# Performance work log

Hardware: AMD Instinct MI355X
Metric: run time of the kernel (lower is better)

The kernel has to match this reference:

```python
import jax, jax.numpy as jnp
import numpy as np

D_MODEL = 1024
D_FFN = 2048
WINDOW = 64
EPS = 1e-6


def rmsnorm(x, w):
    rms = jnp.sqrt(jnp.mean(x * x, axis=-1, keepdims=True) + EPS)
    return x / rms * w


def setup_inputs() -> dict:
    key = jax.random.key(0)
    ks = jax.random.split(key, 9)
    s = 0.02
    return {
        "x": jax.random.normal(ks[0], (4, 2048, D_MODEL), dtype=jnp.float32),
        "norm1_w": jnp.ones((D_MODEL,), dtype=jnp.float32),
        "norm2_w": jnp.ones((D_MODEL,), dtype=jnp.float32),
        "Wq": jax.random.normal(ks[1], (D_MODEL, D_MODEL), dtype=jnp.float32) * s,
        "Wk": jax.random.normal(ks[2], (D_MODEL, D_MODEL), dtype=jnp.float32) * s,
        "Wv": jax.random.normal(ks[3], (D_MODEL, D_MODEL), dtype=jnp.float32) * s,
        "Wo": jax.random.normal(ks[4], (D_MODEL, D_MODEL), dtype=jnp.float32) * s,
        "W1": jax.random.normal(ks[5], (D_MODEL, D_FFN), dtype=jnp.float32) * s,
        "W2": jax.random.normal(ks[6], (D_FFN, D_MODEL), dtype=jnp.float32) * s,
        "W3": jax.random.normal(ks[7], (D_MODEL, D_FFN), dtype=jnp.float32) * s,
    }


def reference(x, norm1_w, norm2_w, Wq, Wk, Wv, Wo, W1, W2, W3):
    B, T, D = x.shape
    scale = D ** (-0.5)
    residual = x
    xn = rmsnorm(x, norm1_w)
    q = xn @ Wq  # [B,T,D]
    k = xn @ Wk
    v = xn @ Wv
    # causal local-window mask: attend iff 0 <= i-j < WINDOW
    rows = jnp.arange(T)[:, None]
    cols = jnp.arange(T)[None, :]
    mask = (cols <= rows) & (rows - cols < WINDOW)  # [T,T] bool
    scores = jnp.einsum("bid,bjd->bij", q, k) * scale
    scores = jnp.where(mask[None], scores, -jnp.inf)
    weights = jax.nn.softmax(scores, axis=-1)
    attended = jnp.einsum("bij,bjd->bid", weights, v)
    x = residual + attended @ Wo
    # SwiGLU FFN
    xn2 = rmsnorm(x, norm2_w)
    ffn = (jax.nn.silu(xn2 @ W1) * (xn2 @ W3)) @ W2
    return x + ffn
```

## Files before the change

kernel.cpp:

```cpp
#include <hip/hip_runtime.h>
#include <hip/hip_bf16.h>

typedef __attribute__((ext_vector_type(8))) short bf16x8;
typedef __attribute__((ext_vector_type(4))) float f32x4;

__device__ __forceinline__ short to_bf16s(float f) {
    union { __hip_bfloat16 h; short s; } u;
    u.h = __float2bfloat16(f);
    return u.s;
}

__device__ __forceinline__ float bf16s_to_f(short s) {
    union { float f; unsigned u; } cv;
    cv.u = ((unsigned)(unsigned short)s) << 16;
    return cv.f;
}

__device__ __forceinline__ void load_lds16(const void* g, void* l) {
    __builtin_amdgcn_global_load_lds((const __attribute__((address_space(1))) void*)g,
                                     (__attribute__((address_space(3))) void*)l, 16, 0, 0);
}

__global__ __launch_bounds__(256)
void transpose_all(const float* __restrict__ Wq, const float* __restrict__ Wk,
                   const float* __restrict__ Wv, const float* __restrict__ Wo,
                   const float* __restrict__ W1, const float* __restrict__ W3,
                   const float* __restrict__ W2,
                   short* __restrict__ WqT, short* __restrict__ WkT,
                   short* __restrict__ WvT, short* __restrict__ WoT,
                   short* __restrict__ W1T, short* __restrict__ W3T,
                   short* __restrict__ W2T) {
    __shared__ float tile[32][33];
    const int bid = blockIdx.x;
    const float* src; short* dst; int K, N, tl;
    if (bid < 4096) {
        const int wi = bid >> 10; tl = bid & 1023;
        src = wi == 0 ? Wq : wi == 1 ? Wk : wi == 2 ? Wv : Wo;
        dst = wi == 0 ? WqT : wi == 1 ? WkT : wi == 2 ? WvT : WoT;
        K = 1024; N = 1024;
    } else if (bid < 8192) {
        const int wi = (bid - 4096) >> 11; tl = (bid - 4096) & 2047;
        src = wi ? W3 : W1; dst = wi ? W3T : W1T;
        K = 1024; N = 2048;
    } else {
        tl = bid - 8192; src = W2; dst = W2T;
        K = 2048; N = 1024;
    }
    const int nx = N >> 5;
    const int n0 = (tl % nx) * 32, k0 = (tl / nx) * 32;
    const int t = threadIdx.x;
    {
        const int lr = t >> 3, lc = (t & 7) * 4;
        float4 v = *(const float4*)&src[(long)(k0 + lr) * N + n0 + lc];
        tile[lr][lc] = v.x; tile[lr][lc + 1] = v.y;
        tile[lr][lc + 2] = v.z; tile[lr][lc + 3] = v.w;
    }
    __syncthreads();
    {
        const int nr = t >> 3, kc = (t & 7) * 4;
        short4 o;
        o.x = to_bf16s(tile[kc][nr]);
        o.y = to_bf16s(tile[kc + 1][nr]);
        o.z = to_bf16s(tile[kc + 2][nr]);
        o.w = to_bf16s(tile[kc + 3][nr]);
        *(short4*)&dst[(long)(n0 + nr) * K + k0 + kc] = o;
    }
}

__global__ __launch_bounds__(256)
void rmsnorm_kernel(const float* __restrict__ x, const float* __restrict__ wt,
                    short* __restrict__ out) {
    const int D = 1024;
    const long row = blockIdx.x;
    const int t = threadIdx.x;
    float4 v = ((const float4*)(x + row * D))[t];
    float ss = v.x * v.x + v.y * v.y + v.z * v.z + v.w * v.w;
    #pragma unroll
    for (int off = 32; off; off >>= 1) ss += __shfl_xor(ss, off);
    __shared__ float red[4];
    if ((t & 63) == 0) red[t >> 6] = ss;
    __syncthreads();
    ss = red[0] + red[1] + red[2] + red[3];
    const float inv = rsqrtf(ss * (1.0f / 1024.0f) + 1e-6f);
    float4 wv = ((const float4*)wt)[t];
    short4 o;
    o.x = to_bf16s(v.x * inv * wv.x);
    o.y = to_bf16s(v.y * inv * wv.y);
    o.z = to_bf16s(v.z * inv * wv.z);
    o.w = to_bf16s(v.w * inv * wv.w);
    *(short4*)&out[row * D + t * 4] = o;
}

#define MFMA16(MB, NB, BREG)                                                   \
    __builtin_amdgcn_s_barrier();                                              \
    asm volatile("s_waitcnt lgkmcnt(0)" ::: "memory");                         \
    __builtin_amdgcn_sched_barrier(0);                                         \
    __builtin_amdgcn_s_setprio(1);                                             \
    _Pragma("unroll")                                                          \
    for (int m_ = 0; m_ < 4; ++m_)                                             \
        _Pragma("unroll")                                                      \
        for (int n_ = 0; n_ < 2; ++n_) {                                       \
            acc[(MB) + m_][(NB) + n_] = __builtin_amdgcn_mfma_f32_16x16x32_bf16( \
                a[m_][0], BREG[n_][0], acc[(MB) + m_][(NB) + n_], 0, 0, 0);    \
            acc[(MB) + m_][(NB) + n_] = __builtin_amdgcn_mfma_f32_16x16x32_bf16( \
                a[m_][1], BREG[n_][1], acc[(MB) + m_][(NB) + n_], 0, 0, 0);    \
        }                                                                      \
    __builtin_amdgcn_s_setprio(0);                                             \
    __builtin_amdgcn_s_barrier();

#define READA(BUF, MG)                                                         \
    _Pragma("unroll")                                                          \
    for (int m_ = 0; m_ < 4; ++m_) {                                           \
        const int rih_ = ((MG) * 4 + m_) * 16 + lm;                            \
        const int rb_ = ((BUF) * 2 + wr) * 16384 + rih_ * 128;                 \
        a[m_][0] = *(const bf16x8*)&lds[rb_ + ((lk * 16) ^ sw)];               \
        a[m_][1] = *(const bf16x8*)&lds[rb_ + ((64 + lk * 16) ^ sw)];          \
    }

#define READB(BUF, NH, ARR)                                                    \
    _Pragma("unroll")                                                          \
    for (int n_ = 0; n_ < 2; ++n_) {                                           \
        const int rih_ = (wc & 1) * 64 + ((NH) * 2 + n_) * 16 + lm;            \
        const int rb_ = 65536 + ((BUF) * 2 + (wc >> 1)) * 16384 + rih_ * 128;  \
        ARR[n_][0] = *(const bf16x8*)&lds[rb_ + ((lk * 16) ^ sw)];             \
        ARR[n_][1] = *(const bf16x8*)&lds[rb_ + ((64 + lk * 16) ^ sw)];        \
    }

template<int EPI>
__global__ __launch_bounds__(512, 2)
void gemm256(const short* __restrict__ A, const short* __restrict__ B0,
             const short* __restrict__ aux, const float* __restrict__ res,
             void* __restrict__ outp, short* __restrict__ outp2,
             int M, int N, int K) {
    __shared__ __align__(16) char lds[131072];

    const int t = threadIdx.x;
    const int lane = t & 63, w = t >> 6;
    const int wr = w >> 2, wc = w & 3;
    const int lm = lane & 15, lk = lane >> 4;
    const int sw = (lm & 7) << 4;

    const int nbn = N >> 8;
    const int nwg = gridDim.x;
    const int chunk = nwg >> 3;
    const int logical = (blockIdx.x & 7) * chunk + (blockIdx.x >> 3);
    const int bm = logical / nbn, bn = logical - (logical / nbn) * nbn;

    const long Kb = (long)K * 2;
    const char* Ab = (const char*)A;
    const char* Bb = (const char*)B0;

    long srcA[2][2], srcB[2][2];
    {
        const int rowp = t >> 3;
        const int cbx = (t & 7) * 16;
        const int swz = ((t >> 3) & 7) << 4;
        #pragma unroll
        for (int h = 0; h < 2; ++h)
            #pragma unroll
            for (int c = 0; c < 2; ++c) {
                srcA[h][c] = (long)(bm * 256 + h * 128 + c * 64 + rowp) * Kb + (cbx ^ swz);
                srcB[h][c] = (long)(bn * 256 + h * 128 + c * 64 + rowp) * Kb + (cbx ^ swz);
            }
    }
    auto stA = [&](int kt, int h) {
        const int buf = kt & 1;
        #pragma unroll
        for (int c = 0; c < 2; ++c)
            load_lds16(Ab + srcA[h][c] + (long)kt * 128,
                       &lds[(buf * 2 + h) * 16384 + c * 8192 + t * 16]);
    };
    auto stB = [&](int kt, int h) {
        const int buf = kt & 1;
        #pragma unroll
        for (int c = 0; c < 2; ++c)
            load_lds16(Bb + srcB[h][c] + (long)kt * 128,
                       &lds[65536 + (buf * 2 + h) * 16384 + c * 8192 + t * 16]);
    };

    f32x4 acc[8][4] = {};
    bf16x8 a[4][2], b0[2][2], b1[2][2];
    const int nt = K >> 6;

    stB(0, 0); stB(0, 1); stA(0, 0); stA(0, 1); stB(1, 0); stB(1, 1);
    asm volatile("s_waitcnt vmcnt(4)" ::: "memory");
    __builtin_amdgcn_s_barrier();

    for (int kt0 = 0; kt0 < nt; kt0 += 2) {
        const int kt1 = kt0 + 1;
        const bool pf = (kt0 + 2) < nt;

        READA(0, 0); READB(0, 0, b0);
        stA(kt1, 0);
        MFMA16(0, 0, b0)
        READB(0, 1, b1);
        stA(kt1, 1);
        MFMA16(0, 2, b1)
        READA(0, 1);
        if (pf) stB(kt0 + 2, 0);
        MFMA16(4, 2, b1)
        if (pf) { stB(kt0 + 2, 1); asm volatile("s_waitcnt vmcnt(4)" ::: "memory"); }
        else    { asm volatile("s_waitcnt vmcnt(0)" ::: "memory"); }
        MFMA16(4, 0, b0)
        READA(1, 0); READB(1, 0, b0);
        if (pf) stA(kt0 + 2, 0);
        MFMA16(0, 0, b0)
        READB(1, 1, b1);
        if (pf) stA(kt0 + 2, 1);
        MFMA16(0, 2, b1)
        READA(1, 1);
        if (pf) stB(kt1 + 2, 0);
        MFMA16(4, 2, b1)
        if (pf) { stB(kt1 + 2, 1); asm volatile("s_waitcnt vmcnt(4)" ::: "memory"); }
        else    { asm volatile("s_waitcnt vmcnt(0)" ::: "memory"); }
        MFMA16(4, 0, b0)
    }

    #pragma unroll
    for (int mf = 0; mf < 8; ++mf)
      #pragma unroll
      for (int nf = 0; nf < 4; ++nf)
        #pragma unroll
        for (int r = 0; r < 4; ++r) {
            const int grow = bm * 256 + wr * 128 + mf * 16 + lk * 4 + r;
            const int gcol = bn * 256 + wc * 64 + nf * 16 + lm;
            const float v = acc[mf][nf][r];
            if constexpr (EPI == 0) {
                ((short*)outp)[(long)grow * N + gcol] = to_bf16s(v);
            } else if constexpr (EPI == 2) {
                const long i = (long)grow * N + gcol;
                ((float*)outp)[i] = res[i] + v;
            } else if constexpr (EPI == 4) {
                const long i = (long)grow * N + gcol;
                const float g = bf16s_to_f(aux[i]);
                const float sws = g / (1.f + __expf(-g));
                ((short*)outp)[i] = to_bf16s(sws * v);
            } else {
                if (gcol < 2048)
                    ((short*)outp)[(long)grow * 2048 + gcol] = to_bf16s(v);
                else
                    outp2[(long)(gcol - 2048) * 8192 + grow] = to_bf16s(v);
            }
        }
}

__global__ __launch_bounds__(128)
void attn_kernel(const short* __restrict__ Q, const short* __restrict__ Km,
                 int ldq, const short* __restrict__ VT, short* __restrict__ att) {
    const int T = 2048, D = 1024, Mtot = 8192;
    const int bid = blockIdx.x;
    const int b = bid >> 6;
    const int q0 = (bid & 63) << 5;
    const long qrow0 = (long)b * T + q0;
    const int t = threadIdx.x, lane = t & 63, w = t >> 6;

    __shared__ short Qs[32 * 32];
    __shared__ short Ks[96 * 32];
    __shared__ float S_lds[32][100];
    __shared__ short P_lds[32 * 96];
    __shared__ short VTs[128 * 96];

    f32x4 s[6] = {};
    const int trow = t >> 2, tk8 = (t & 3) * 8;
    for (int kt = 0; kt < 32; ++kt) {
        const int k0 = kt << 5;
        load_lds16(Q + (qrow0 + trow) * ldq + k0 + tk8, &Qs[t * 8]);
        #pragma unroll
        for (int s2 = 0; s2 < 3; ++s2) {
            const int krow = s2 * 32 + trow;
            int j = q0 - 64 + krow; if (j < 0) j = 0;
            load_lds16(Km + ((long)b * T + j) * ldq + k0 + tk8, &Ks[(s2 * 128 + t) * 8]);
        }
        __syncthreads();
        const int ko = (lane >> 4) * 8;
        const bf16x8 aq = *(const bf16x8*)&Qs[(w * 16 + (lane & 15)) * 32 + ko];
        #pragma unroll
        for (int n = 0; n < 6; ++n) {
            const bf16x8 bk = *(const bf16x8*)&Ks[(n * 16 + (lane & 15)) * 32 + ko];
            s[n] = __builtin_amdgcn_mfma_f32_16x16x32_bf16(aq, bk, s[n], 0, 0, 0);
        }
        __syncthreads();
    }
    #pragma unroll
    for (int n = 0; n < 6; ++n)
        #pragma unroll
        for (int r = 0; r < 4; ++r)
            S_lds[w * 16 + ((lane >> 4) << 2) + r][n * 16 + (lane & 15)] = s[n][r] * 0.03125f;
    __syncthreads();

    {
        const int row = t >> 2, c0 = (t & 3) * 24;
        float e[24];
        float mx = -1e30f;
        #pragma unroll
        for (int c = 0; c < 24; ++c) {
            const int kj = c0 + c;
            const bool valid = (kj > row) && (kj <= row + 64) && (q0 - 64 + kj >= 0);
            const float sv = valid ? S_lds[row][kj] : -1e30f;
            e[c] = sv;
            mx = fmaxf(mx, sv);
        }
        mx = fmaxf(mx, __shfl_xor(mx, 1));
        mx = fmaxf(mx, __shfl_xor(mx, 2));
        float sum = 0.f;
        #pragma unroll
        for (int c = 0; c < 24; ++c) {
            const float ev = (e[c] > -1e29f) ? __expf(e[c] - mx) : 0.f;
            e[c] = ev; sum += ev;
        }
        sum += __shfl_xor(sum, 1);
        sum += __shfl_xor(sum, 2);
        const float inv = 1.f / sum;
        #pragma unroll
        for (int c = 0; c < 24; ++c)
            P_lds[row * 96 + c0 + c] = to_bf16s(e[c] * inv);
    }
    __syncthreads();

    bf16x8 pa[3];
    {
        const int ko = (lane >> 4) * 8;
        #pragma unroll
        for (int kc = 0; kc < 3; ++kc)
            pa[kc] = *(const bf16x8*)&P_lds[(w * 16 + (lane & 15)) * 96 + kc * 32 + ko];
    }
    for (int dc = 0; dc < 8; ++dc) {
        #pragma unroll
        for (int s2 = 0; s2 < 12; ++s2) {
            const int idx = s2 * 128 + t;
            const int dr = idx / 12, c = idx - dr * 12;
            int j = q0 - 64 + c * 8; if (j < 0) j = 0;
            load_lds16(VT + (long)(dc * 128 + dr) * Mtot + b * T + j, &VTs[idx * 8]);
        }
        __syncthreads();
        f32x4 o[8] = {};
        const int ko = (lane >> 4) * 8;
        #pragma unroll
        for (int kc = 0; kc < 3; ++kc)
            #pragma unroll
            for (int n = 0; n < 8; ++n) {
                const bf16x8 vb = *(const bf16x8*)&VTs[(n * 16 + (lane & 15)) * 96 + kc * 32 + ko];
                o[n] = __builtin_amdgcn_mfma_f32_16x16x32_bf16(pa[kc], vb, o[n], 0, 0, 0);
            }
        __syncthreads();
        #pragma unroll
        for (int n = 0; n < 8; ++n)
            #pragma unroll
            for (int r = 0; r < 4; ++r) {
                const long grow = qrow0 + w * 16 + ((lane >> 4) << 2) + r;
                const int gcol = dc * 128 + n * 16 + (lane & 15);
                att[grow * D + gcol] = to_bf16s(o[n][r]);
            }
    }
}

extern "C" void kernel_launch(void* const* d_in, const int* in_sizes, int n_in,
                              void* d_out, int out_size, void* d_ws, size_t ws_size,
                              hipStream_t stream) {
    const float* x   = (const float*)d_in[0];
    const float* n1w = (const float*)d_in[1];
    const float* n2w = (const float*)d_in[2];
    const float* Wq  = (const float*)d_in[3];
    const float* Wk  = (const float*)d_in[4];
    const float* Wv  = (const float*)d_in[5];
    const float* Wo  = (const float*)d_in[6];
    const float* W1  = (const float*)d_in[7];
    const float* W2  = (const float*)d_in[8];
    const float* W3  = (const float*)d_in[9];

    const int M = 8192;
    char* ws = (char*)d_ws;
    size_t off = 0;
    auto alloc = [&](size_t bytes) { void* p = ws + off; off += (bytes + 255) & ~(size_t)255; return p; };

    short* xn1 = (short*)alloc((size_t)M * 1024 * 2);
    short* qk  = (short*)alloc((size_t)M * 2048 * 2);
    short* vT  = (short*)alloc((size_t)M * 1024 * 2);
    float* x2  = (float*)alloc((size_t)M * 1024 * 4);
    short* WqT = (short*)alloc((size_t)1024 * 1024 * 2);
    short* WkT = (short*)alloc((size_t)1024 * 1024 * 2);
    short* WvT = (short*)alloc((size_t)1024 * 1024 * 2);
    short* WoT = (short*)alloc((size_t)1024 * 1024 * 2);
    short* W1T = (short*)alloc((size_t)2048 * 1024 * 2);
    short* W3T = (short*)alloc((size_t)2048 * 1024 * 2);
    short* W2T = (short*)alloc((size_t)1024 * 2048 * 2);
    short* att = xn1;
    short* xn2 = qk;
    short* g1  = qk + (size_t)M * 1024;

    transpose_all<<<10240, 256, 0, stream>>>(Wq, Wk, Wv, Wo, W1, W3, W2,
                                             WqT, WkT, WvT, WoT, W1T, W3T, W2T);

    rmsnorm_kernel<<<M, 256, 0, stream>>>(x, n1w, xn1);
    gemm256<5><<<384, 512, 0, stream>>>(xn1, WqT, nullptr, nullptr, qk, vT, M, 3072, 1024);
    attn_kernel<<<256, 128, 0, stream>>>(qk, qk + 1024, 2048, vT, att);
    gemm256<2><<<128, 512, 0, stream>>>(att, WoT, nullptr, x, x2, nullptr, M, 1024, 1024);
    rmsnorm_kernel<<<M, 256, 0, stream>>>(x2, n2w, xn2);
    gemm256<0><<<256, 512, 0, stream>>>(xn2, W1T, nullptr, nullptr, g1, nullptr, M, 2048, 1024);
    gemm256<4><<<256, 512, 0, stream>>>(xn2, W3T, g1, nullptr, g1, nullptr, M, 2048, 1024);
    gemm256<2><<<128, 512, 0, stream>>>(g1, W2T, nullptr, x2, (float*)d_out, nullptr, M, 1024, 2048);
}
```

Baseline: 317.3 us.

## Fuse W1/W3 GEMMs with interleaved weights, add 256x128 GEMM, double-buffer attention

W1 and W3 are interleaved row by row into one transposed weight, so a single GEMM yields gate and up values in adjacent columns. A lane shuffle pairs them for the SiLU product, which removes one GEMM launch and the round-trip of g1 through memory. A new 256x128-tile GEMM with a three-stage LDS pipeline replaces the 256x256 one for the QKV, Wo and W2 projections, doubling the workgroup count so more CUs are busy. The attention kernel double-buffers its Q/K and V tile loads to overlap global loads with MFMA work. It also drops a sched_barrier and the memory clobber on the waitcnt, which may let the compiler reorder around the LDS wait.

Result: faster. 305.0 us (-3.9%).

```diff
diff --git a/kernel.cpp b/kernel.cpp
--- a/kernel.cpp
+++ b/kernel.cpp
@@ -8,12 +8,6 @@
     union { __hip_bfloat16 h; short s; } u;
     u.h = __float2bfloat16(f);
     return u.s;
-}
-
-__device__ __forceinline__ float bf16s_to_f(short s) {
-    union { float f; unsigned u; } cv;
-    cv.u = ((unsigned)(unsigned short)s) << 16;
-    return cv.f;
 }
 
 __device__ __forceinline__ void load_lds16(const void* g, void* l) {
@@ -28,11 +22,10 @@
                    const float* __restrict__ W2,
                    short* __restrict__ WqT, short* __restrict__ WkT,
                    short* __restrict__ WvT, short* __restrict__ WoT,
-                   short* __restrict__ W1T, short* __restrict__ W3T,
-                   short* __restrict__ W2T) {
+                   short* __restrict__ W13T, short* __restrict__ W2T) {
     __shared__ float tile[32][33];
     const int bid = blockIdx.x;
-    const float* src; short* dst; int K, N, tl;
+    const float* src; short* dst; int K, N, tl, rs = 1, ro = 0;
     if (bid < 4096) {
         const int wi = bid >> 10; tl = bid & 1023;
         src = wi == 0 ? Wq : wi == 1 ? Wk : wi == 2 ? Wv : Wo;
@@ -40,7 +33,7 @@
         K = 1024; N = 1024;
     } else if (bid < 8192) {
         const int wi = (bid - 4096) >> 11; tl = (bid - 4096) & 2047;
-        src = wi ? W3 : W1; dst = wi ? W3T : W1T;
+        src = wi ? W3 : W1; dst = W13T; rs = 2; ro = wi;
         K = 1024; N = 2048;
     } else {
         tl = bid - 8192; src = W2; dst = W2T;
@@ -63,7 +56,7 @@
         o.y = to_bf16s(tile[kc + 1][nr]);
         o.z = to_bf16s(tile[kc + 2][nr]);
         o.w = to_bf16s(tile[kc + 3][nr]);
-        *(short4*)&dst[(long)(n0 + nr) * K + k0 + kc] = o;
+        *(short4*)&dst[(long)((n0 + nr) * rs + ro) * K + k0 + kc] = o;
     }
 }
 
@@ -93,8 +86,7 @@
 
 #define MFMA16(MB, NB, BREG)                                                   \
     __builtin_amdgcn_s_barrier();                                              \
-    asm volatile("s_waitcnt lgkmcnt(0)" ::: "memory");                         \
-    __builtin_amdgcn_sched_barrier(0);                                         \
+    asm volatile("s_waitcnt lgkmcnt(0)");                                      \
     __builtin_amdgcn_s_setprio(1);                                             \
     _Pragma("unroll")                                                          \
     for (int m_ = 0; m_ < 4; ++m_)                                             \
@@ -108,30 +100,135 @@
     __builtin_amdgcn_s_setprio(0);                                             \
     __builtin_amdgcn_s_barrier();
 
-#define READA(BUF, MG)                                                         \
+#define RA1(BUF)                                                               \
     _Pragma("unroll")                                                          \
     for (int m_ = 0; m_ < 4; ++m_) {                                           \
-        const int rih_ = ((MG) * 4 + m_) * 16 + lm;                            \
-        const int rb_ = ((BUF) * 2 + wr) * 16384 + rih_ * 128;                 \
+        const int rb_ = (BUF) * 32768 + (wr * 64 + m_ * 16 + lm) * 128;        \
         a[m_][0] = *(const bf16x8*)&lds[rb_ + ((lk * 16) ^ sw)];               \
         a[m_][1] = *(const bf16x8*)&lds[rb_ + ((64 + lk * 16) ^ sw)];          \
     }
-
-#define READB(BUF, NH, ARR)                                                    \
+#define RB1(BUF, NG, ARR)                                                      \
     _Pragma("unroll")                                                          \
     for (int n_ = 0; n_ < 2; ++n_) {                                           \
-        const int rih_ = (wc & 1) * 64 + ((NH) * 2 + n_) * 16 + lm;            \
-        const int rb_ = 65536 + ((BUF) * 2 + (wc >> 1)) * 16384 + rih_ * 128;  \
+        const int rb_ = 98304 + (BUF) * 16384 +                                \
+                        (wc * 64 + ((NG) * 2 + n_) * 16 + lm) * 128;           \
         ARR[n_][0] = *(const bf16x8*)&lds[rb_ + ((lk * 16) ^ sw)];             \
         ARR[n_][1] = *(const bf16x8*)&lds[rb_ + ((64 + lk * 16) ^ sw)];        \
     }
 
 template<int EPI>
 __global__ __launch_bounds__(512, 2)
-void gemm256(const short* __restrict__ A, const short* __restrict__ B0,
-             const short* __restrict__ aux, const float* __restrict__ res,
-             void* __restrict__ outp, short* __restrict__ outp2,
-             int M, int N, int K) {
+void gemm128r(const short* __restrict__ A, const short* __restrict__ B0,
+              const float* __restrict__ res, void* __restrict__ outp,
+              short* __restrict__ outp2, int M, int N, int K) {
+    __shared__ __align__(16) char lds[147456];
+
+    const int t = threadIdx.x;
+    const int lane = t & 63, w = t >> 6;
+    const int wr = w >> 1, wc = w & 1;
+    const int lm = lane & 15, lk = lane >> 4;
+    const int sw = (lm & 7) << 4;
+
+    const int nbn = N >> 7;
+    const int chunk = gridDim.x >> 3;
+    const int logical = (blockIdx.x & 7) * chunk + (blockIdx.x >> 3);
+    const int bm = logical / nbn, bn = logical - (logical / nbn) * nbn;
+
+    const long Kb = (long)K * 2;
+    const char* Ab = (const char*)A;
+    const char* Bb = (const char*)B0;
+
+    long srcA[2][2], srcB[2];
+    {
+        const int rowp = t >> 3;
+        const int cbx = (t & 7) * 16;
+        const int swz = ((t >> 3) & 7) << 4;
+        #pragma unroll
+        for (int h = 0; h < 2; ++h)
+            #pragma unroll
+            for (int c = 0; c < 2; ++c)
+                srcA[h][c] = (long)(bm * 256 + h * 128 + c * 64 + rowp) * Kb + (cbx ^ swz);
+        #pragma unroll
+        for (int c = 0; c < 2; ++c)
+            srcB[c] = (long)(bn * 128 + c * 64 + rowp) * Kb + (cbx ^ swz);
+    }
+    auto stA = [&](int kt, int h, int buf) {
+        #pragma unroll
+        for (int c = 0; c < 2; ++c)
+            load_lds16(Ab + srcA[h][c] + (long)kt * 128,
+                       &lds[buf * 32768 + h * 16384 + c * 8192 + t * 16]);
+    };
+    auto stB = [&](int kt, int buf) {
+        #pragma unroll
+        for (int c = 0; c < 2; ++c)
+            load_lds16(Bb + srcB[c] + (long)kt * 128,
+                       &lds[98304 + buf * 16384 + c * 8192 + t * 16]);
+    };
+
+    f32x4 acc[4][4] = {};
+    bf16x8 a[4][2], b0[2][2], b1[2][2];
+    const int nt = K >> 6;
+
+    stA(0, 0, 0); stA(0, 1, 0); stB(0, 0);
+    stA(1, 0, 1); stA(1, 1, 1); stB(1, 1);
+    asm volatile("s_waitcnt vmcnt(6)" ::: "memory");
+    __builtin_amdgcn_s_barrier();
+
+    int cur = 0, stg = 2;
+    for (int kt = 0; kt < nt; ++kt) {
+        const bool pf = (kt + 2) < nt;
+        RA1(cur); RB1(cur, 0, b0);
+        if (pf) { stA(kt + 2, 0, stg); stA(kt + 2, 1, stg); }
+        MFMA16(0, 0, b0)
+        RB1(cur, 1, b1);
+        if (pf) stB(kt + 2, stg);
+        if (kt + 1 < nt) asm volatile("s_waitcnt vmcnt(6)" ::: "memory");
+        else             asm volatile("s_waitcnt vmcnt(0)" ::: "memory");
+        MFMA16(0, 2, b1)
+        cur = (cur == 2) ? 0 : cur + 1;
+        stg = (stg == 2) ? 0 : stg + 1;
+    }
+
+    #pragma unroll
+    for (int mf = 0; mf < 4; ++mf)
+      #pragma unroll
+      for (int nf = 0; nf < 4; ++nf)
+        #pragma unroll
+        for (int r = 0; r < 4; ++r) {
+            const int grow = bm * 256 + wr * 64 + mf * 16 + lk * 4 + r;
+            const int gcol = bn * 128 + wc * 64 + nf * 16 + lm;
+            const float v = acc[mf][nf][r];
+            if constexpr (EPI == 2) {
+                const long i = (long)grow * N + gcol;
+                ((float*)outp)[i] = res[i] + v;
+            } else {
+                if (gcol < 2048)
+                    ((short*)outp)[(long)grow * 2048 + gcol] = to_bf16s(v);
+                else
+                    outp2[(long)(gcol - 2048) * 8192 + grow] = to_bf16s(v);
+            }
+        }
+}
+
+#define RA2(BUF, MG)                                                           \
+    _Pragma("unroll")                                                          \
+    for (int m_ = 0; m_ < 4; ++m_) {                                           \
+        const int rb_ = ((BUF) * 2 + wr) * 16384 + (((MG) * 4 + m_) * 16 + lm) * 128; \
+        a[m_][0] = *(const bf16x8*)&lds[rb_ + ((lk * 16) ^ sw)];               \
+        a[m_][1] = *(const bf16x8*)&lds[rb_ + ((64 + lk * 16) ^ sw)];          \
+    }
+#define RB2(BUF, NH, ARR)                                                      \
+    _Pragma("unroll")                                                          \
+    for (int n_ = 0; n_ < 2; ++n_) {                                           \
+        const int rb_ = 65536 + ((BUF) * 2 + (wc >> 1)) * 16384 +              \
+                        ((wc & 1) * 64 + ((NH) * 2 + n_) * 16 + lm) * 128;     \
+        ARR[n_][0] = *(const bf16x8*)&lds[rb_ + ((lk * 16) ^ sw)];             \
+        ARR[n_][1] = *(const bf16x8*)&lds[rb_ + ((64 + lk * 16) ^ sw)];        \
+    }
+
+__global__ __launch_bounds__(512, 2)
+void gemm256f(const short* __restrict__ A, const short* __restrict__ B0,
+              short* __restrict__ outp, int M, int N, int K) {
     __shared__ __align__(16) char lds[131072];
 
     const int t = threadIdx.x;
@@ -141,8 +238,7 @@
     const int sw = (lm & 7) << 4;
 
     const int nbn = N >> 8;
-    const int nwg = gridDim.x;
-    const int chunk = nwg >> 3;
+    const int chunk = gridDim.x >> 3;
     const int logical = (blockIdx.x & 7) * chunk + (blockIdx.x >> 3);
     const int bm = logical / nbn, bn = logical - (logical / nbn) * nbn;
 
@@ -186,36 +282,35 @@
     asm volatile("s_waitcnt vmcnt(4)" ::: "memory");
     __builtin_amdgcn_s_barrier();
 
-    for (int kt0 = 0; kt0 < nt; kt0 += 2) {
-        const int kt1 = kt0 + 1;
-        const bool pf = (kt0 + 2) < nt;
-
-        READA(0, 0); READB(0, 0, b0);
-        stA(kt1, 0);
+    for (int u = 0; u < nt; u += 2) {
+        const bool pf = (u + 2) < nt;
+        RA2(0, 0); RB2(0, 0, b0);
+        stA(u + 1, 0);
         MFMA16(0, 0, b0)
-        READB(0, 1, b1);
-        stA(kt1, 1);
+        RB2(0, 1, b1);
+        stA(u + 1, 1);
         MFMA16(0, 2, b1)
-        READA(0, 1);
-        if (pf) stB(kt0 + 2, 0);
+        RA2(0, 1);
+        if (pf) stB(u + 2, 0);
         MFMA16(4, 2, b1)
-        if (pf) { stB(kt0 + 2, 1); asm volatile("s_waitcnt vmcnt(4)" ::: "memory"); }
+        if (pf) { stB(u + 2, 1); asm volatile("s_waitcnt vmcnt(4)" ::: "memory"); }
         else    { asm volatile("s_waitcnt vmcnt(0)" ::: "memory"); }
         MFMA16(4, 0, b0)
-        READA(1, 0); READB(1, 0, b0);
-        if (pf) stA(kt0 + 2, 0);
+        RA2(1, 0); RB2(1, 0, b0);
+        if (pf) stA(u + 2, 0);
         MFMA16(0, 0, b0)
-        READB(1, 1, b1);
-        if (pf) stA(kt0 + 2, 1);
+        RB2(1, 1, b1);
+        if (pf) stA(u + 2, 1);
         MFMA16(0, 2, b1)
-        READA(1, 1);
-        if (pf) stB(kt1 + 2, 0);
+        RA2(1, 1);
+        if (pf) stB(u + 3, 0);
         MFMA16(4, 2, b1)
-        if (pf) { stB(kt1 + 2, 1); asm volatile("s_waitcnt vmcnt(4)" ::: "memory"); }
+        if (pf) { stB(u + 3, 1); asm volatile("s_waitcnt vmcnt(4)" ::: "memory"); }
         else    { asm volatile("s_waitcnt vmcnt(0)" ::: "memory"); }
         MFMA16(4, 0, b0)
     }
 
+    const int NH = N >> 1;
     #pragma unroll
     for (int mf = 0; mf < 8; ++mf)
       #pragma unroll
@@ -225,21 +320,10 @@
             const int grow = bm * 256 + wr * 128 + mf * 16 + lk * 4 + r;
             const int gcol = bn * 256 + wc * 64 + nf * 16 + lm;
             const float v = acc[mf][nf][r];
-            if constexpr (EPI == 0) {
-                ((short*)outp)[(long)grow * N + gcol] = to_bf16s(v);
-            } else if constexpr (EPI == 2) {
-                const long i = (long)grow * N + gcol;
-                ((float*)outp)[i] = res[i] + v;
-            } else if constexpr (EPI == 4) {
-                const long i = (long)grow * N + gcol;
-                const float g = bf16s_to_f(aux[i]);
-                const float sws = g / (1.f + __expf(-g));
-                ((short*)outp)[i] = to_bf16s(sws * v);
-            } else {
-                if (gcol < 2048)
-                    ((short*)outp)[(long)grow * 2048 + gcol] = to_bf16s(v);
-                else
-                    outp2[(long)(gcol - 2048) * 8192 + grow] = to_bf16s(v);
+            const float g3 = __shfl_xor(v, 1);
+            if (!(lane & 1)) {
+                const float sws = v / (1.f + __expf(-v));
+                outp[(long)grow * NH + (gcol >> 1)] = to_bf16s(sws * g3);
             }
         }
 }
@@ -254,29 +338,35 @@
     const long qrow0 = (long)b * T + q0;
     const int t = threadIdx.x, lane = t & 63, w = t >> 6;
 
-    __shared__ short Qs[32 * 32];
-    __shared__ short Ks[96 * 32];
+    __shared__ short Qs[2][32 * 32];
+    __shared__ short Ks[2][96 * 32];
     __shared__ float S_lds[32][100];
     __shared__ short P_lds[32 * 96];
-    __shared__ short VTs[128 * 96];
-
-    f32x4 s[6] = {};
+    __shared__ short VTs[2][128 * 96];
+
     const int trow = t >> 2, tk8 = (t & 3) * 8;
-    for (int kt = 0; kt < 32; ++kt) {
+    auto stageQK = [&](int kt, int bf) {
         const int k0 = kt << 5;
-        load_lds16(Q + (qrow0 + trow) * ldq + k0 + tk8, &Qs[t * 8]);
+        load_lds16(Q + (qrow0 + trow) * ldq + k0 + tk8, &Qs[bf][t * 8]);
         #pragma unroll
         for (int s2 = 0; s2 < 3; ++s2) {
             const int krow = s2 * 32 + trow;
             int j = q0 - 64 + krow; if (j < 0) j = 0;
-            load_lds16(Km + ((long)b * T + j) * ldq + k0 + tk8, &Ks[(s2 * 128 + t) * 8]);
-        }
-        __syncthreads();
+            load_lds16(Km + ((long)b * T + j) * ldq + k0 + tk8, &Ks[bf][(s2 * 128 + t) * 8]);
+        }
+    };
+
+    f32x4 s[6] = {};
+    stageQK(0, 0);
+    __syncthreads();
+    for (int kt = 0; kt < 32; ++kt) {
+        const int cb = kt & 1;
+        if (kt + 1 < 32) stageQK(kt + 1, cb ^ 1);
         const int ko = (lane >> 4) * 8;
-        const bf16x8 aq = *(const bf16x8*)&Qs[(w * 16 + (lane & 15)) * 32 + ko];
+        const bf16x8 aq = *(const bf16x8*)&Qs[cb][(w * 16 + (lane & 15)) * 32 + ko];
         #pragma unroll
         for (int n = 0; n < 6; ++n) {
-            const bf16x8 bk = *(const bf16x8*)&Ks[(n * 16 + (lane & 15)) * 32 + ko];
+            const bf16x8 bk = *(const bf16x8*)&Ks[cb][(n * 16 + (lane & 15)) * 32 + ko];
             s[n] = __builtin_amdgcn_mfma_f32_16x16x32_bf16(aq, bk, s[n], 0, 0, 0);
         }
         __syncthreads();
@@ -315,31 +405,36 @@
         for (int c = 0; c < 24; ++c)
             P_lds[row * 96 + c0 + c] = to_bf16s(e[c] * inv);
     }
-    __syncthreads();
-
-    bf16x8 pa[3];
-    {
-        const int ko = (lane >> 4) * 8;
-        #pragma unroll
-        for (int kc = 0; kc < 3; ++kc)
-            pa[kc] = *(const bf16x8*)&P_lds[(w * 16 + (lane & 15)) * 96 + kc * 32 + ko];
-    }
-    for (int dc = 0; dc < 8; ++dc) {
+
+    auto stageV = [&](int dc, int bf) {
         #pragma unroll
         for (int s2 = 0; s2 < 12; ++s2) {
             const int idx = s2 * 128 + t;
             const int dr = idx / 12, c = idx - dr * 12;
             int j = q0 - 64 + c * 8; if (j < 0) j = 0;
-            load_lds16(VT + (long)(dc * 128 + dr) * Mtot + b * T + j, &VTs[idx * 8]);
-        }
-        __syncthreads();
+            load_lds16(VT + (long)(dc * 128 + dr) * Mtot + b * T + j, &VTs[bf][idx * 8]);
+        }
+    };
+    stageV(0, 0);
+    __syncthreads();
+
+    bf16x8 pa[3];
+    {
+        const int ko = (lane >> 4) * 8;
+        #pragma unroll
+        for (int kc = 0; kc < 3; ++kc)
+            pa[kc] = *(const bf16x8*)&P_lds[(w * 16 + (lane & 15)) * 96 + kc * 32 + ko];
+    }
+    for (int dc = 0; dc < 8; ++dc) {
+        const int cb = dc & 1;
+        if (dc + 1 < 8) stageV(dc + 1, cb ^ 1);
         f32x4 o[8] = {};
         const int ko = (lane >> 4) * 8;
         #pragma unroll
         for (int kc = 0; kc < 3; ++kc)
             #pragma unroll
             for (int n = 0; n < 8; ++n) {
-                const bf16x8 vb = *(const bf16x8*)&VTs[(n * 16 + (lane & 15)) * 96 + kc * 32 + ko];
+                const bf16x8 vb = *(const bf16x8*)&VTs[cb][(n * 16 + (lane & 15)) * 96 + kc * 32 + ko];
                 o[n] = __builtin_amdgcn_mfma_f32_16x16x32_bf16(pa[kc], vb, o[n], 0, 0, 0);
             }
         __syncthreads();
@@ -381,22 +476,20 @@
     short* WkT = (short*)alloc((size_t)1024 * 1024 * 2);
     short* WvT = (short*)alloc((size_t)1024 * 1024 * 2);
     short* WoT = (short*)alloc((size_t)1024 * 1024 * 2);
-    short* W1T = (short*)alloc((size_t)2048 * 1024 * 2);
-    short* W3T = (short*)alloc((size_t)2048 * 1024 * 2);
+    short* W13T= (short*)alloc((size_t)4096 * 1024 * 2);
     short* W2T = (short*)alloc((size_t)1024 * 2048 * 2);
     short* att = xn1;
     short* xn2 = qk;
-    short* g1  = qk + (size_t)M * 1024;
+    short* h   = qk + (size_t)M * 1024;
 
     transpose_all<<<10240, 256, 0, stream>>>(Wq, Wk, Wv, Wo, W1, W3, W2,
-                                             WqT, WkT, WvT, WoT, W1T, W3T, W2T);
+                                             WqT, WkT, WvT, WoT, W13T, W2T);
 
     rmsnorm_kernel<<<M, 256, 0, stream>>>(x, n1w, xn1);
-    gemm256<5><<<384, 512, 0, stream>>>(xn1, WqT, nullptr, nullptr, qk, vT, M, 3072, 1024);
+    gemm128r<5><<<768, 512, 0, stream>>>(xn1, WqT, nullptr, qk, vT, M, 3072, 1024);
     attn_kernel<<<256, 128, 0, stream>>>(qk, qk + 1024, 2048, vT, att);
-    gemm256<2><<<128, 512, 0, stream>>>(att, WoT, nullptr, x, x2, nullptr, M, 1024, 1024);
+    gemm128r<2><<<256, 512, 0, stream>>>(att, WoT, x, x2, nullptr, M, 1024, 1024);
     rmsnorm_kernel<<<M, 256, 0, stream>>>(x2, n2w, xn2);
-    gemm256<0><<<256, 512, 0, stream>>>(xn2, W1T, nullptr, nullptr, g1, nullptr, M, 2048, 1024);
-    gemm256<4><<<256, 512, 0, stream>>>(xn2, W3T, g1, nullptr, g1, nullptr, M, 2048, 1024);
-    gemm256<2><<<128, 512, 0, stream>>>(g1, W2T, nullptr, x2, (float*)d_out, nullptr, M, 1024, 2048);
-}
+    gemm256f<<<512, 512, 0, stream>>>(xn2, W13T, h, M, 4096, 1024);
+    gemm128r<2><<<256, 512, 0, stream>>>(h, W2T, x2, (float*)d_out, nullptr, M, 1024, 2048);
+}
```
